# Optimization experiments

Measured on AMD Instinct MI355X. Metric: run time of the kernel, lower is better.

The kernel has to match this reference:

```python
import jax, jax.numpy as jnp
import numpy as np

B, N, P = 256, 12, 66
DN = 1024   # node_feature_size
DE = 1024   # edge_feature_size
D = 512     # message_size
DIMS = [3 * D, 1024, 512]  # shared trunk dims; heads differ only in out classes
C_LR, C_CR, C_MR = 9, 3, 5


def _mlp(x, Ws, bs):
    # ReLU MLP, no activation on final layer (eval mode: dropout is identity)
    for i, (W, b) in enumerate(zip(Ws, bs)):
        x = x @ W + b
        if i < len(Ws) - 1:
            x = jax.nn.relu(x)
    return x


def _head_params(key, out_dim):
    dims = DIMS + [out_dim]
    Ws, bs = [], []
    for i in range(len(dims) - 1):
        key, k = jax.random.split(key)
        Ws.append(jax.random.normal(k, (dims[i], dims[i + 1]), jnp.float32) * (1.0 / np.sqrt(dims[i])))
        bs.append(jnp.zeros((dims[i + 1],), jnp.float32))
    return Ws, bs


def setup_inputs() -> dict:
    key = jax.random.key(0)
    ks = jax.random.split(key, 12)
    inp = {
        'node_features': jax.random.normal(ks[0], (B, N, DN), jnp.float32),
        'edge_features': jax.random.normal(ks[1], (B, N, N, DE), jnp.float32),
        'edge_embeddings': jax.random.normal(ks[2], (B, N, N, D), jnp.float32),
        'pairs': jax.random.randint(ks[3], (B, P, 2), 0, N),
        'num_rels': jax.random.randint(ks[4], (B,), 0, P + 1),
        'W_node': jax.random.normal(ks[5], (DN, D), jnp.float32) * (1.0 / np.sqrt(DN)),
        'b_node': jnp.zeros((D,), jnp.float32),
        'W_edge': jax.random.normal(ks[6], (DE, D), jnp.float32) * (1.0 / np.sqrt(DE)),
        'b_edge': jnp.zeros((D,), jnp.float32),
    }
    for name, cdim, k in (('lr', C_LR, ks[7]), ('cr', C_CR, ks[8]), ('mr', C_MR, ks[9])):
        Ws, bs = _head_params(k, cdim)
        for i in range(3):
            inp[f'{name}_W{i}'] = Ws[i]
            inp[f'{name}_b{i}'] = bs[i]
    return inp


def reference(node_features, edge_features, edge_embeddings, pairs, num_rels,
              W_node, b_node, W_edge, b_edge,
              lr_W0, lr_b0, lr_W1, lr_b1, lr_W2, lr_b2,
              cr_W0, cr_b0, cr_W1, cr_b1, cr_W2, cr_b2,
              mr_W0, mr_b0, mr_W1, mr_b1, mr_W2, mr_b2):
    # feature resize linears
    nf = node_features @ W_node + b_node        # [B,N,D]
    ef = edge_features @ W_edge + b_edge        # [B,N,N,D]

    # vectorized make_classifier_inputs
    i0, i1 = pairs[..., 0], pairs[..., 1]       # [B,P]
    bidx = jnp.arange(nf.shape[0])[:, None]     # [B,1]
    n1 = nf[bidx, i0]                           # [B,P,D]
    n2 = nf[bidx, i1]                           # [B,P,D]
    emb_mean = 0.5 * (edge_embeddings[bidx, i0, i1] + edge_embeddings[bidx, i1, i0])
    feat_mean = 0.5 * (ef[bidx, i0, i1] + ef[bidx, i1, i0])
    e = 0.5 * (emb_mean + feat_mean)            # [B,P,D]
    ci = jnp.concatenate([n1, n2, e], axis=-1)  # [B,P,3D]

    # rows i >= num_rels[b] stay zero (preallocated-zeros semantics)
    valid = (jnp.arange(ci.shape[1])[None, :] < num_rels[:, None])[..., None]
    ci = jnp.where(valid, ci, jnp.zeros((), ci.dtype))

    lr = _mlp(ci, [lr_W0, lr_W1, lr_W2], [lr_b0, lr_b1, lr_b2])
    cr = _mlp(ci, [cr_W0, cr_W1, cr_W2], [cr_b0, cr_b1, cr_b2])
    mr = _mlp(ci, [mr_W0, mr_W1, mr_W2], [mr_b0, mr_b1, mr_b2])
    return lr, cr, mr
```

## Files before the change

### kernel.cpp

```cpp
#include <hip/hip_runtime.h>
#include <stdint.h>

#define BB 256
#define NNODE 12
#define PP 66
#define DNF 1024
#define DEF 1024
#define DD 512
#define MROWS (BB*PP)
#define MNODE (BB*NNODE)
#define MTILES (MROWS/128)

typedef __attribute__((ext_vector_type(8))) short s16x8;
typedef __attribute__((ext_vector_type(4))) float f32x4;
typedef __attribute__((ext_vector_type(8))) unsigned short u16x8;

__device__ __forceinline__ unsigned short f2bf(float f) {
  union { float f; unsigned u; } v; v.f = f;
  return (unsigned short)((v.u + 0x7FFFu + ((v.u >> 16) & 1u)) >> 16);
}
__device__ __forceinline__ float bf2f(unsigned short h) {
  union { unsigned u; float f; } v; v.u = ((unsigned)h) << 16;
  return v.f;
}

__device__ __forceinline__ void gll16(const void* g, void* l) {
  __builtin_amdgcn_global_load_lds(
      (const __attribute__((address_space(1))) void*)g,
      (__attribute__((address_space(3))) void*)l, 16, 0, 0);
}

__global__ __launch_bounds__(256) void k_front(
    const int* __restrict__ nrels, int* __restrict__ offs,
    int* __restrict__ Mv, int2* __restrict__ nodes,
    float* __restrict__ h1part,
    const float* __restrict__ node, unsigned short* __restrict__ node_bf,
    const float* __restrict__ W_node, unsigned short* __restrict__ WnT,
    const float* __restrict__ W_edge, unsigned short* __restrict__ WeT,
    const float* __restrict__ W0a, const float* __restrict__ W0b,
    const float* __restrict__ W0c, unsigned short* __restrict__ W0T,
    const float* __restrict__ W1a, const float* __restrict__ W1b,
    const float* __restrict__ W1c, unsigned short* __restrict__ W1T,
    const float* __restrict__ w2a, const float* __restrict__ w2b,
    const float* __restrict__ w2c,
    const float* __restrict__ b2a, const float* __restrict__ b2b,
    const float* __restrict__ b2c,
    unsigned short* __restrict__ W2T, float* __restrict__ b2pad,
    const float* __restrict__ b0a, const float* __restrict__ b0b,
    const float* __restrict__ b0c, float* __restrict__ b0cat,
    const float* __restrict__ b1a, const float* __restrict__ b1b,
    const float* __restrict__ b1c, float* __restrict__ b1cat,
    const float* __restrict__ b_node, const float* __restrict__ b_edge,
    float* __restrict__ b_ne) {
  __shared__ float tile[64][65];
  const int bid = blockIdx.x, t = threadIdx.x;
  if (bid < 24) {
    const int h = bid >> 3, c = bid & 7;
    const float* b0 = h == 0 ? b0a : (h == 1 ? b0b : b0c);
    const float* W1 = h == 0 ? W1a : (h == 1 ? W1b : W1c);
    const int k0 = c * 128;
    float acc0 = 0.f, acc1 = 0.f;
#pragma unroll 8
    for (int kk = 0; kk < 128; ++kk) {
      const int k = k0 + kk;
      const float bv = fmaxf(b0[k], 0.f);
      acc0 += bv * W1[(size_t)k * 512 + t];
      acc1 += bv * W1[(size_t)k * 512 + t + 256];
    }
    h1part[(size_t)bid * 512 + t] = acc0;
    h1part[(size_t)bid * 512 + t + 256] = acc1;
  } else if (bid == 24) {
    __shared__ int s[256];
    const int val = nrels[t];
    s[t] = val;
    __syncthreads();
    for (int d = 1; d < 256; d <<= 1) {
      int x = (t >= d) ? s[t - d] : 0;
      __syncthreads();
      s[t] += x;
      __syncthreads();
    }
    offs[t] = s[t] - val;
    __syncthreads();
    const int total = s[255];
    if (t == 0) *Mv = total;
    if (t < 128) {
      int cr = total + t;
      if (cr < MROWS) nodes[cr] = make_int2(0, 0);
    }
  } else if (bid < 3097) {
    int i = (bid - 25) * 256 + t;
    float4 v = ((const float4*)node)[i];
    ushort4 o;
    o.x = f2bf(v.x); o.y = f2bf(v.y); o.z = f2bf(v.z); o.w = f2bf(v.w);
    ((ushort4*)node_bf)[i] = o;
  } else if (bid < 4889) {
    int tau = bid - 3097;
    const float* src; unsigned short* dst; int K, N;
    if (tau < 128)       { src = W_node; dst = WnT; K = 1024; N = 512; }
    else if (tau < 256)  { src = W_edge; dst = WeT; K = 1024; N = 512; tau -= 128; }
    else if (tau < 1408) {
      int hh = (tau - 256) / 384; tau = (tau - 256) % 384;
      src = hh == 0 ? W0a : (hh == 1 ? W0b : W0c);
      dst = W0T + (size_t)hh * 1024 * 1536; K = 1536; N = 1024;
    } else {
      int hh = (tau - 1408) / 128; tau = (tau - 1408) % 128;
      src = hh == 0 ? W1a : (hh == 1 ? W1b : W1c);
      dst = W1T + (size_t)hh * 512 * 1024; K = 1024; N = 512;
    }
    const int ntn = N >> 6;
    const int kb = (tau / ntn) * 64, nb = (tau % ntn) * 64;
    const int tx = t & 15, ty = t >> 4;
#pragma unroll
    for (int i = 0; i < 4; i++) {
      float4 v = *(const float4*)&src[(size_t)(kb + ty + 16 * i) * N + nb + tx * 4];
      tile[ty + 16 * i][tx * 4 + 0] = v.x;
      tile[ty + 16 * i][tx * 4 + 1] = v.y;
      tile[ty + 16 * i][tx * 4 + 2] = v.z;
      tile[ty + 16 * i][tx * 4 + 3] = v.w;
    }
    __syncthreads();
    const int wx = t & 7, wy = t >> 3;
#pragma unroll
    for (int i = 0; i < 2; i++) {
      const int n = wy + 32 * i;
      u16x8 o;
#pragma unroll
      for (int j = 0; j < 8; j++) o[j] = f2bf(tile[wx * 8 + j][n]);
      *(u16x8*)&dst[(size_t)(nb + n) * K + kb + wx * 8] = o;
    }
  } else if (bid < 5657) {
    int e = bid - 4889;
    int h = e >> 8, blk = e & 255;
    const int C = (h == 0) ? 9 : ((h == 1) ? 3 : 5);
    const float* W2 = (h == 0) ? w2a : ((h == 1) ? w2b : w2c);
    const float* b2 = (h == 0) ? b2a : ((h == 1) ? b2b : b2c);
    int idx = blk * 256 + t;
    int n = idx >> 9, k = idx & 511;
    W2T[(size_t)h * 65536 + idx] = (n < C) ? f2bf(W2[(size_t)k * C + n]) : (unsigned short)0;
    if (blk == 0 && t < 128)
      b2pad[h * 128 + t] = (t < C) ? b2[t] : 0.f;
  } else if (bid < 5669) {
    int j = bid - 5657;
    const float* b0 = (j < 4) ? b0a : (j < 8 ? b0b : b0c);
    b0cat[j * 256 + t] = b0[(j & 3) * 256 + t];
  } else if (bid < 5675) {
    int j = bid - 5669;
    const float* b1 = (j < 2) ? b1a : (j < 4 ? b1b : b1c);
    b1cat[j * 256 + t] = b1[(j & 1) * 256 + t];
  } else {
    int idx = (bid - 5675) * 256 + t;
    b_ne[idx] = (idx < 512) ? b_node[idx] : b_edge[idx - 512];
  }
}

__global__ __launch_bounds__(256) void k_gather_fin(
    const float* __restrict__ EF, const float* __restrict__ EE,
    const int* __restrict__ pairs, const int* __restrict__ nrels,
    const int* __restrict__ offs,
    unsigned short* __restrict__ efm, unsigned short* __restrict__ emb,
    int2* __restrict__ nodes, int* __restrict__ rmap,
    const float* __restrict__ h1part,
    const float* __restrict__ b1a, const float* __restrict__ b1b,
    const float* __restrict__ b1c,
    const float* __restrict__ w2a, const float* __restrict__ w2b,
    const float* __restrict__ w2c,
    const float* __restrict__ b2a, const float* __restrict__ b2b,
    const float* __restrict__ b2c, float* __restrict__ outc) {
  const int bid = blockIdx.x, t = threadIdx.x;
  if (bid == MROWS) {
    __shared__ float red[9];
    for (int h = 0; h < 3; ++h) {
      const float* b1 = h == 0 ? b1a : (h == 1 ? b1b : b1c);
      const float* W2 = h == 0 ? w2a : (h == 1 ? w2b : w2c);
      const float* b2 = h == 0 ? b2a : (h == 1 ? b2b : b2c);
      const int C = h == 0 ? 9 : (h == 1 ? 3 : 5);
      const int obase = h == 0 ? 0 : (h == 1 ? 9 : 12);
      if (t < 9) red[t] = 0.f;
      float s0 = b1[t], s1 = b1[t + 256];
#pragma unroll
      for (int cc = 0; cc < 8; ++cc) {
        s0 += h1part[(size_t)(h * 8 + cc) * 512 + t];
        s1 += h1part[(size_t)(h * 8 + cc) * 512 + t + 256];
      }
      const float hv0 = fmaxf(s0, 0.f), hv1 = fmaxf(s1, 0.f);
      __syncthreads();
      float p[9] = {0.f, 0.f, 0.f, 0.f, 0.f, 0.f, 0.f, 0.f, 0.f};
#pragma unroll
      for (int c = 0; c < 9; ++c)
        if (c < C) p[c] = hv0 * W2[(size_t)t * C + c] + hv1 * W2[(size_t)(t + 256) * C + c];
#pragma unroll
      for (int c = 0; c < 9; ++c)
#pragma unroll
        for (int off = 32; off; off >>= 1) p[c] += __shfl_xor(p[c], off);
      if ((t & 63) == 0)
        for (int c = 0; c < C; ++c) atomicAdd(&red[c], p[c]);
      __syncthreads();
      if (t < C) outc[obase + t] = red[t] + b2[t];
      __syncthreads();
    }
    return;
  }
  int r = bid;
  int b = r / PP, p = r - b * PP;
  if (p >= nrels[b]) return;
  const int cr = offs[b] + p;
  int i0 = pairs[r * 2 + 0], i1 = pairs[r * 2 + 1];
  if (t == 0) {
    nodes[cr] = make_int2(b * NNODE + i0, b * NNODE + i1);
    rmap[cr] = r;
  }
  const float4* e01 = (const float4*)(EF + ((size_t)((b * NNODE + i0) * NNODE + i1)) * DEF);
  const float4* e10 = (const float4*)(EF + ((size_t)((b * NNODE + i1) * NNODE + i0)) * DEF);
  float4 a = e01[t], c = e10[t];
  ushort4 o;
  o.x = f2bf(0.5f * (a.x + c.x));
  o.y = f2bf(0.5f * (a.y + c.y));
  o.z = f2bf(0.5f * (a.z + c.z));
  o.w = f2bf(0.5f * (a.w + c.w));
  ((ushort4*)(efm + (size_t)cr * DEF))[t] = o;
  const float2* g01 = (const float2*)(EE + ((size_t)((b * NNODE + i0) * NNODE + i1)) * DD);
  const float2* g10 = (const float2*)(EE + ((size_t)((b * NNODE + i1) * NNODE + i0)) * DD);
  float2 x = g01[t], y = g10[t];
  ushort2 eo;
  eo.x = f2bf(0.25f * (x.x + y.x));
  eo.y = f2bf(0.25f * (x.y + y.y));
  ((ushort2*)(emb + (size_t)cr * DD))[t] = eo;
}

template <int EPI>
__global__ __launch_bounds__(256) void k_gemm(
    const unsigned short* __restrict__ A, int ldA,
    const unsigned short* __restrict__ BT, int ldB, int K,
    int Ntiles,
    const float* __restrict__ bias,
    unsigned short* __restrict__ outb, int ldo,
    const unsigned short* __restrict__ em,
    const int* __restrict__ Mvp,
    unsigned short* __restrict__ ci,
    int blocksPerHead, long long aHeadOff, long long bHeadOff,
    long long oHeadOff, int biasHeadOff,
    const int2* __restrict__ nodes,
    const unsigned short* __restrict__ nfa,
    const unsigned short* __restrict__ nfb,
    const int* __restrict__ rmap) {
  __shared__ __align__(16) unsigned short sm[16384];
  char* smc = (char*)sm;
  const int t = threadIdx.x;
  int bid = blockIdx.x;

  if constexpr (EPI == 6) {
    if (bid >= 2 * blocksPerHead) {
      const float* oc = (const float*)nfa;
      float* out = (float*)nfb;
      const int e = (bid - 2 * blocksPerHead) * 256 + t;
      if (e < MROWS * 17) {
        int c;
        if (e < MROWS * 9) c = e % 9;
        else if (e < MROWS * 12) c = 9 + (e - MROWS * 9) % 3;
        else c = 12 + (e - MROWS * 12) % 5;
        out[e] = oc[c];
      }
      return;
    }
  }

  const int l = t & 63, w = t >> 6;
  const int wm = w >> 1, wn = w & 1;

  int head = 0;
  unsigned short* outp = outb;
  if constexpr (EPI == 3) {
    head = bid / MTILES;
    bid -= head * MTILES;
    A += (size_t)head * MROWS * DD;
    BT += (size_t)head * 128 * DD;
    bias += head * 128;
  } else {
    if (blocksPerHead > 0) {
      head = bid / blocksPerHead;
      bid -= head * blocksPerHead;
      A += (long long)head * aHeadOff;
      BT += (long long)head * bHeadOff;
      bias += head * biasHeadOff;
      outp = outb + (long long)head * oHeadOff;
    }
  }
  const int tn = bid % Ntiles, tm = bid / Ntiles;

  int Mv = MROWS;
  if (Mvp) Mv = *Mvp;
  if constexpr (EPI == 6) { if (head == 0) Mv = MNODE; }
  if (Mvp) {
    if (tm * 128 >= Mv) return;
  }

  const int lrow = l >> 3;
  const int scol = (l & 7) ^ lrow;
  const unsigned short* Ap = A + (size_t)(tm * 128 + w * 8 + lrow) * ldA + scol * 8;
  const unsigned short* Bp = BT + (size_t)(tn * 128 + w * 8 + lrow) * ldB + scol * 8;

  f32x4 acc[4][4] = {};
  const int hi = l >> 4, l15 = l & 15, l7 = l & 7;
  const int nk = K >> 6;

  for (int kt = 0; kt < nk; ++kt) {
#pragma unroll
    for (int c = 0; c < 4; ++c) {
      gll16(Ap + (size_t)c * 32 * ldA, smc + c * 4096 + w * 1024);
      gll16(Bp + (size_t)c * 32 * ldB, smc + 16384 + c * 4096 + w * 1024);
    }
    __syncthreads();
#pragma unroll
    for (int kk = 0; kk < 2; ++kk) {
      const int cb = (((kk << 2) + hi) ^ l7) << 4;
      s16x8 af[4], bfr[4];
#pragma unroll
      for (int m = 0; m < 4; m++)
        af[m] = *(const s16x8*)(smc + (wm * 64 + m * 16 + l15) * 128 + cb);
#pragma unroll
      for (int n = 0; n < 4; n++)
        bfr[n] = *(const s16x8*)(smc + 16384 + (wn * 64 + n * 16 + l15) * 128 + cb);
#pragma unroll
      for (int m = 0; m < 4; m++)
#pragma unroll
        for (int n = 0; n < 4; n++)
          asm volatile("v_mfma_f32_16x16x32_bf16 %0, %1, %2, %0"
                       : "+v"(acc[m][n])
                       : "v"(af[m]), "v"(bfr[n]));
    }
    __syncthreads();
    Ap += 64;
    Bp += 64;
  }
  asm volatile("s_nop 7\n\ts_nop 7\n\ts_nop 7" :::);

  if constexpr (EPI == 5) {
    const int se_r = t >> 4;
    const int se_ch = t & 15;
#pragma unroll
    for (int it = 0; it < 8; ++it) {
      const int rr = se_r + (it << 4);
      const int2 nn = nodes[tm * 128 + rr];
      union { unsigned short s[8]; unsigned long long q[2]; } ov;
      u16x8 va = *(const u16x8*)&nfa[(size_t)nn.x * 3072 + tn * 128 + se_ch * 8];
      u16x8 vb = *(const u16x8*)&nfb[(size_t)nn.y * 3072 + tn * 128 + se_ch * 8];
#pragma unroll
      for (int j = 0; j < 8; ++j)
        ov.s[j] = f2bf(bf2f(va[j]) + bf2f(vb[j]));
      const int sch = se_ch ^ ((rr >> 2) & 7);
      *(unsigned long long*)(smc + rr * 256 + (sch << 4)) = ov.q[0];
      *(unsigned long long*)(smc + rr * 256 + (sch << 4) + 8) = ov.q[1];
    }
    __syncthreads();
  }

  const int gr_base = tm * 128 + wm * 64 + (hi << 2);
  const int gc_base = tn * 128 + wn * 64 + l15;
  const int lr_base = wm * 64 + (hi << 2);
  const int lc_base = wn * 64 + l15;

  int Cc = 0; size_t obase = 0;
  if constexpr (EPI == 3) {
    Cc = (head == 0) ? 9 : ((head == 1) ? 3 : 5);
    obase = (head == 0) ? 0 : ((head == 1) ? (size_t)MROWS * 9 : (size_t)MROWS * 12);
  }

#pragma unroll
  for (int n = 0; n < 4; n++) {
    const int gc = gc_base + n * 16;
    const float bv = (EPI == 4) ? 0.f : bias[gc];
#pragma unroll
    for (int m = 0; m < 4; m++) {
#pragma unroll
      for (int i = 0; i < 4; i++) {
        const int gr = gr_base + m * 16 + i;
        float v = acc[m][n][i] + bv;
        if constexpr (EPI == 0 || EPI == 4) {
          outp[(size_t)gr * ldo + gc] = f2bf(v);
        } else if constexpr (EPI == 2) {
          outp[(size_t)gr * ldo + gc] = f2bf(v > 0.f ? v : 0.f);
        } else if constexpr (EPI == 5) {
          const int lr = lr_base + m * 16 + i;
          const int lc = lc_base + n * 16;
          const int rch = (lc >> 3) ^ ((lr >> 2) & 7);
          v += bf2f(*(const unsigned short*)(smc + lr * 256 + (rch << 4) + (lc & 7) * 2));
          outp[(size_t)gr * ldo + gc] = f2bf(v > 0.f ? v : 0.f);
        } else if constexpr (EPI == 6) {
          if (head == 0) {
            outp[(size_t)gr * ldo + gc] = f2bf(v);
          } else {
            float e = bf2f(em[(size_t)gr * DD + gc]) + 0.5f * v;
            ci[(size_t)gr * DD + gc] = f2bf(e);
          }
        } else {
          if (gc < Cc && gr < Mv)
            ((float*)outb)[obase + (size_t)rmap[gr] * Cc + gc] = v;
        }
      }
    }
  }
}

extern "C" void kernel_launch(void* const* d_in, const int* in_sizes, int n_in,
                              void* d_out, int out_size, void* d_ws, size_t ws_size,
                              hipStream_t stream) {
  const float* node   = (const float*)d_in[0];
  const float* EF     = (const float*)d_in[1];
  const float* EE     = (const float*)d_in[2];
  const int*   pairs  = (const int*)d_in[3];
  const int*   nrels  = (const int*)d_in[4];
  const float* W_node = (const float*)d_in[5];
  const float* b_node = (const float*)d_in[6];
  const float* W_edge = (const float*)d_in[7];
  const float* b_edge = (const float*)d_in[8];
  const float* hW0[3] = {(const float*)d_in[9],  (const float*)d_in[15], (const float*)d_in[21]};
  const float* hb0[3] = {(const float*)d_in[10], (const float*)d_in[16], (const float*)d_in[22]};
  const float* hW1[3] = {(const float*)d_in[11], (const float*)d_in[17], (const float*)d_in[23]};
  const float* hb1[3] = {(const float*)d_in[12], (const float*)d_in[18], (const float*)d_in[24]};
  const float* hW2[3] = {(const float*)d_in[13], (const float*)d_in[19], (const float*)d_in[25]};
  const float* hb2[3] = {(const float*)d_in[14], (const float*)d_in[20], (const float*)d_in[26]};

  char* ws = (char*)d_ws;
  size_t off = 0;
  auto alloc = [&](size_t bytes) {
    char* p = ws + off;
    off += (bytes + 255) & ~(size_t)255;
    return p;
  };
  unsigned short* WnT    = (unsigned short*)alloc((size_t)512 * 1024 * 2);
  unsigned short* WeT    = (unsigned short*)alloc((size_t)512 * 1024 * 2);
  unsigned short* W0T    = (unsigned short*)alloc((size_t)3072 * 1536 * 2);
  unsigned short* W1T    = (unsigned short*)alloc((size_t)3 * 512 * 1024 * 2);
  unsigned short* W2T    = (unsigned short*)alloc((size_t)3 * 128 * 512 * 2);
  float*          b2pad  = (float*)alloc((size_t)3 * 128 * 4);
  float*          b0cat  = (float*)alloc((size_t)3072 * 4);
  float*          b1cat  = (float*)alloc((size_t)1536 * 4);
  float*          b_ne   = (float*)alloc((size_t)1024 * 4);
  int2*           nodes  = (int2*)alloc((size_t)MROWS * 8);
  int*            offs   = (int*)alloc((size_t)256 * 4);
  int*            Mv     = (int*)alloc(256);
  int*            rmap   = (int*)alloc((size_t)MROWS * 4);
  float*          outc   = (float*)alloc((size_t)32 * 4);
  float*          h1part = (float*)alloc((size_t)24 * 512 * 4);
  size_t zoneA = off;
  unsigned short* efm = (unsigned short*)alloc((size_t)MROWS * DEF * 2);
  unsigned short* EMb = (unsigned short*)alloc((size_t)MROWS * DD * 2);
  unsigned short* ci_e = (unsigned short*)alloc((size_t)MROWS * DD * 2);
  size_t zoneC = off;
  unsigned short* node_bf = (unsigned short*)alloc((size_t)MNODE * DNF * 2);
  unsigned short* nf      = (unsigned short*)alloc((size_t)MNODE * DD * 2);
  unsigned short* nfa   = (unsigned short*)(ws + zoneA);
  unsigned short* nfb   = nfa + (size_t)MNODE * 3072;
  unsigned short* h1    = (unsigned short*)(ws + zoneA);
  unsigned short* h0big = (unsigned short*)(ws + zoneC);

  k_front<<<5679, 256, 0, stream>>>(nrels, offs, Mv, nodes, h1part,
      node, node_bf, W_node, WnT, W_edge, WeT,
      hW0[0], hW0[1], hW0[2], W0T, hW1[0], hW1[1], hW1[2], W1T,
      hW2[0], hW2[1], hW2[2], hb2[0], hb2[1], hb2[2], W2T, b2pad,
      hb0[0], hb0[1], hb0[2], b0cat, hb1[0], hb1[1], hb1[2], b1cat,
      b_node, b_edge, b_ne);
  k_gather_fin<<<MROWS + 1, 256, 0, stream>>>(EF, EE, pairs, nrels, offs,
      efm, EMb, nodes, rmap, h1part,
      hb1[0], hb1[1], hb1[2], hW2[0], hW2[1], hW2[2],
      hb2[0], hb2[1], hb2[2], outc);

  k_gemm<6><<<2 * MTILES * 4 + (MROWS * 17 + 255) / 256, 256, 0, stream>>>(
      node_bf, 1024, WnT, 1024, 1024, 4, b_ne, nf, 512,
      EMb, Mv, ci_e, MTILES * 4,
      (long long)(efm - node_bf), (long long)512 * 1024,
      (long long)(ci_e - nf), 512,
      nullptr, (const unsigned short*)outc, (const unsigned short*)d_out, nullptr);

  k_gemm<4><<<2 * (MNODE / 128) * 24, 256, 0, stream>>>(
      nf, 512, W0T, 1536, 512, 24, nullptr, nfa, 3072,
      nullptr, nullptr, nullptr, (MNODE / 128) * 24,
      0, 512, (long long)MNODE * 3072, 0, nullptr, nullptr, nullptr, nullptr);

  k_gemm<5><<<MTILES * 24, 256, 0, stream>>>(
      ci_e, 512, W0T + 1024, 1536, 512, 24, b0cat, h0big, 3072,
      nullptr, Mv, nullptr, 0, 0, 0, 0, 0, nodes, nfa, nfb, nullptr);

  k_gemm<2><<<3 * MTILES * 4, 256, 0, stream>>>(
      h0big, 3072, W1T, 1024, 1024, 4, b1cat, h1, 512,
      nullptr, Mv, nullptr, MTILES * 4,
      1024, (long long)512 * 1024, (long long)MROWS * DD, 512,
      nullptr, nullptr, nullptr, nullptr);

  k_gemm<3><<<3 * MTILES, 256, 0, stream>>>(
      h1, 512, W2T, 512, 512, 1, b2pad, (unsigned short*)d_out, 0,
      nullptr, Mv, nullptr, 0, 0, 0, 0, 0, nullptr, nullptr, nullptr, rmap);
}
```

Before: 201.4 us.

## Fuse node-resize GEMM into gather kernel and merge edge and W0 node GEMMs

```diff
diff --git a/kernel.cpp b/kernel.cpp
--- a/kernel.cpp
+++ b/kernel.cpp
@@ -154,7 +154,158 @@
   }
 }
 
-__global__ __launch_bounds__(256) void k_gather_fin(
+template <int EPI>
+__device__ __forceinline__ void gemm_body(
+    unsigned short* sm,
+    const unsigned short* __restrict__ A, int ldA,
+    const unsigned short* __restrict__ BT, int ldB, int K,
+    int Ntiles,
+    const float* __restrict__ bias,
+    unsigned short* __restrict__ outb, int ldo,
+    const unsigned short* __restrict__ em,
+    const int* __restrict__ Mvp,
+    unsigned short* __restrict__ ci,
+    int blocksPerHead, long long aHeadOff, long long bHeadOff,
+    long long oHeadOff, int biasHeadOff,
+    const int2* __restrict__ nodes,
+    const unsigned short* __restrict__ nfa,
+    const unsigned short* __restrict__ nfb,
+    const int* __restrict__ rmap, int bid) {
+  char* smc = (char*)sm;
+  const int t = threadIdx.x;
+  const int l = t & 63, w = t >> 6;
+  const int wm = w >> 1, wn = w & 1;
+
+  int head = 0;
+  unsigned short* outp = outb;
+  if constexpr (EPI == 3) {
+    head = bid / MTILES;
+    bid -= head * MTILES;
+    A += (size_t)head * MROWS * DD;
+    BT += (size_t)head * 128 * DD;
+    bias += head * 128;
+  } else {
+    if (blocksPerHead > 0) {
+      head = bid / blocksPerHead;
+      bid -= head * blocksPerHead;
+      A += (long long)head * aHeadOff;
+      BT += (long long)head * bHeadOff;
+      bias += head * biasHeadOff;
+      outp = outb + (long long)head * oHeadOff;
+    }
+  }
+  const int tn = bid % Ntiles, tm = bid / Ntiles;
+
+  int Mv = MROWS;
+  if (Mvp) {
+    Mv = *Mvp;
+    if (tm * 128 >= Mv) return;
+  }
+
+  const int lrow = l >> 3;
+  const int scol = (l & 7) ^ lrow;
+  const unsigned short* Ap = A + (size_t)(tm * 128 + w * 8 + lrow) * ldA + scol * 8;
+  const unsigned short* Bp = BT + (size_t)(tn * 128 + w * 8 + lrow) * ldB + scol * 8;
+
+  f32x4 acc[4][4] = {};
+  const int hi = l >> 4, l15 = l & 15, l7 = l & 7;
+  const int nk = K >> 6;
+
+  for (int kt = 0; kt < nk; ++kt) {
+#pragma unroll
+    for (int c = 0; c < 4; ++c) {
+      gll16(Ap + (size_t)c * 32 * ldA, smc + c * 4096 + w * 1024);
+      gll16(Bp + (size_t)c * 32 * ldB, smc + 16384 + c * 4096 + w * 1024);
+    }
+    __syncthreads();
+#pragma unroll
+    for (int kk = 0; kk < 2; ++kk) {
+      const int cb = (((kk << 2) + hi) ^ l7) << 4;
+      s16x8 af[4], bfr[4];
+#pragma unroll
+      for (int m = 0; m < 4; m++)
+        af[m] = *(const s16x8*)(smc + (wm * 64 + m * 16 + l15) * 128 + cb);
+#pragma unroll
+      for (int n = 0; n < 4; n++)
+        bfr[n] = *(const s16x8*)(smc + 16384 + (wn * 64 + n * 16 + l15) * 128 + cb);
+#pragma unroll
+      for (int m = 0; m < 4; m++)
+#pragma unroll
+        for (int n = 0; n < 4; n++)
+          asm volatile("v_mfma_f32_16x16x32_bf16 %0, %1, %2, %0"
+                       : "+v"(acc[m][n])
+                       : "v"(af[m]), "v"(bfr[n]));
+    }
+    __syncthreads();
+    Ap += 64;
+    Bp += 64;
+  }
+  asm volatile("s_nop 7\n\ts_nop 7\n\ts_nop 7" :::);
+
+  if constexpr (EPI == 5) {
+    const int se_r = t >> 4;
+    const int se_ch = t & 15;
+#pragma unroll
+    for (int it = 0; it < 8; ++it) {
+      const int rr = se_r + (it << 4);
+      const int2 nn = nodes[tm * 128 + rr];
+      union { unsigned short s[8]; unsigned long long q[2]; } ov;
+      u16x8 va = *(const u16x8*)&nfa[(size_t)nn.x * 3072 + tn * 128 + se_ch * 8];
+      u16x8 vb = *(const u16x8*)&nfb[(size_t)nn.y * 3072 + tn * 128 + se_ch * 8];
+#pragma unroll
+      for (int j = 0; j < 8; ++j)
+        ov.s[j] = f2bf(bf2f(va[j]) + bf2f(vb[j]));
+      const int sch = se_ch ^ ((rr >> 2) & 7);
+      *(unsigned long long*)(smc + rr * 256 + (sch << 4)) = ov.q[0];
+      *(unsigned long long*)(smc + rr * 256 + (sch << 4) + 8) = ov.q[1];
+    }
+    __syncthreads();
+  }
+
+  const int gr_base = tm * 128 + wm * 64 + (hi << 2);
+  const int gc_base = tn * 128 + wn * 64 + l15;
+  const int lr_base = wm * 64 + (hi << 2);
+  const int lc_base = wn * 64 + l15;
+
+  int Cc = 0; size_t obase = 0;
+  if constexpr (EPI == 3) {
+    Cc = (head == 0) ? 9 : ((head == 1) ? 3 : 5);
+    obase = (head == 0) ? 0 : ((head == 1) ? (size_t)MROWS * 9 : (size_t)MROWS * 12);
+  }
+
+#pragma unroll
+  for (int n = 0; n < 4; n++) {
+    const int gc = gc_base + n * 16;
+    const float bv = (EPI == 4) ? 0.f : bias[gc];
+#pragma unroll
+    for (int m = 0; m < 4; m++) {
+#pragma unroll
+      for (int i = 0; i < 4; i++) {
+        const int gr = gr_base + m * 16 + i;
+        float v = acc[m][n][i] + bv;
+        if constexpr (EPI == 0 || EPI == 4) {
+          outp[(size_t)gr * ldo + gc] = f2bf(v);
+        } else if constexpr (EPI == 1) {
+          float e = bf2f(em[(size_t)gr * DD + gc]) + 0.5f * v;
+          ci[(size_t)gr * DD + gc] = f2bf(e);
+        } else if constexpr (EPI == 2) {
+          outp[(size_t)gr * ldo + gc] = f2bf(v > 0.f ? v : 0.f);
+        } else if constexpr (EPI == 5) {
+          const int lr = lr_base + m * 16 + i;
+          const int lc = lc_base + n * 16;
+          const int rch = (lc >> 3) ^ ((lr >> 2) & 7);
+          v += bf2f(*(const unsigned short*)(smc + lr * 256 + (rch << 4) + (lc & 7) * 2));
+          outp[(size_t)gr * ldo + gc] = f2bf(v > 0.f ? v : 0.f);
+        } else {
+          if (gc < Cc && gr < Mv)
+            ((float*)outb)[obase + (size_t)rmap[gr] * Cc + gc] = v;
+        }
+      }
+    }
+  }
+}
+
+__global__ __launch_bounds__(256) void k_gather_nf(
     const float* __restrict__ EF, const float* __restrict__ EE,
     const int* __restrict__ pairs, const int* __restrict__ nrels,
     const int* __restrict__ offs,
@@ -166,10 +317,20 @@
     const float* __restrict__ w2a, const float* __restrict__ w2b,
     const float* __restrict__ w2c,
     const float* __restrict__ b2a, const float* __restrict__ b2b,
-    const float* __restrict__ b2c, float* __restrict__ outc) {
+    const float* __restrict__ b2c, float* __restrict__ outc,
+    const unsigned short* __restrict__ node_bf,
+    const unsigned short* __restrict__ WnT,
+    const float* __restrict__ b_node, unsigned short* __restrict__ nf) {
+  __shared__ __align__(16) unsigned short sm[16384];
   const int bid = blockIdx.x, t = threadIdx.x;
+  if (bid > MROWS) {
+    gemm_body<0>(sm, node_bf, 1024, WnT, 1024, 1024, 4, b_node, nf, 512,
+                 nullptr, nullptr, nullptr, 0, 0, 0, 0, 0,
+                 nullptr, nullptr, nullptr, nullptr, bid - MROWS - 1);
+    return;
+  }
   if (bid == MROWS) {
-    __shared__ float red[9];
+    float* red = (float*)sm;
     for (int h = 0; h < 3; ++h) {
       const float* b1 = h == 0 ? b1a : (h == 1 ? b1b : b1c);
       const float* W2 = h == 0 ? w2a : (h == 1 ? w2b : w2c);
@@ -226,6 +387,37 @@
   eo.x = f2bf(0.25f * (x.x + y.x));
   eo.y = f2bf(0.25f * (x.y + y.y));
   ((ushort2*)(emb + (size_t)cr * DD))[t] = eo;
+}
+
+__global__ __launch_bounds__(256) void k_mid(
+    const unsigned short* __restrict__ efm, const unsigned short* __restrict__ WeT,
+    const float* __restrict__ b_edge,
+    const unsigned short* __restrict__ EMb, const int* __restrict__ Mvp,
+    unsigned short* __restrict__ ci_e,
+    const unsigned short* __restrict__ nf, const unsigned short* __restrict__ W0T,
+    unsigned short* __restrict__ nfa,
+    const float* __restrict__ outc, float* __restrict__ out) {
+  __shared__ __align__(16) unsigned short sm[16384];
+  const int bid = blockIdx.x, t = threadIdx.x;
+  if (bid < 528) {
+    gemm_body<1>(sm, efm, 1024, WeT, 1024, 1024, 4, b_edge, nullptr, 0,
+                 EMb, Mvp, ci_e, 0, 0, 0, 0, 0,
+                 nullptr, nullptr, nullptr, nullptr, bid);
+  } else if (bid < 1680) {
+    gemm_body<4>(sm, nf, 512, W0T, 1536, 512, 24, nullptr, nfa, 3072,
+                 nullptr, nullptr, nullptr, 576,
+                 0, 512, (long long)MNODE * 3072, 0,
+                 nullptr, nullptr, nullptr, nullptr, bid - 528);
+  } else {
+    const int e = (bid - 1680) * 256 + t;
+    if (e < MROWS * 17) {
+      int c;
+      if (e < MROWS * 9) c = e % 9;
+      else if (e < MROWS * 12) c = 9 + (e - MROWS * 9) % 3;
+      else c = 12 + (e - MROWS * 12) % 5;
+      out[e] = outc[c];
+    }
+  }
 }
 
 template <int EPI>
@@ -245,161 +437,9 @@
     const unsigned short* __restrict__ nfb,
     const int* __restrict__ rmap) {
   __shared__ __align__(16) unsigned short sm[16384];
-  char* smc = (char*)sm;
-  const int t = threadIdx.x;
-  int bid = blockIdx.x;
-
-  if constexpr (EPI == 6) {
-    if (bid >= 2 * blocksPerHead) {
-      const float* oc = (const float*)nfa;
-      float* out = (float*)nfb;
-      const int e = (bid - 2 * blocksPerHead) * 256 + t;
-      if (e < MROWS * 17) {
-        int c;
-        if (e < MROWS * 9) c = e % 9;
-        else if (e < MROWS * 12) c = 9 + (e - MROWS * 9) % 3;
-        else c = 12 + (e - MROWS * 12) % 5;
-        out[e] = oc[c];
-      }
-      return;
-    }
-  }
-
-  const int l = t & 63, w = t >> 6;
-  const int wm = w >> 1, wn = w & 1;
-
-  int head = 0;
-  unsigned short* outp = outb;
-  if constexpr (EPI == 3) {
-    head = bid / MTILES;
-    bid -= head * MTILES;
-    A += (size_t)head * MROWS * DD;
-    BT += (size_t)head * 128 * DD;
-    bias += head * 128;
-  } else {
-    if (blocksPerHead > 0) {
-      head = bid / blocksPerHead;
-      bid -= head * blocksPerHead;
-      A += (long long)head * aHeadOff;
-      BT += (long long)head * bHeadOff;
-      bias += head * biasHeadOff;
-      outp = outb + (long long)head * oHeadOff;
-    }
-  }
-  const int tn = bid % Ntiles, tm = bid / Ntiles;
-
-  int Mv = MROWS;
-  if (Mvp) Mv = *Mvp;
-  if constexpr (EPI == 6) { if (head == 0) Mv = MNODE; }
-  if (Mvp) {
-    if (tm * 128 >= Mv) return;
-  }
-
-  const int lrow = l >> 3;
-  const int scol = (l & 7) ^ lrow;
-  const unsigned short* Ap = A + (size_t)(tm * 128 + w * 8 + lrow) * ldA + scol * 8;
-  const unsigned short* Bp = BT + (size_t)(tn * 128 + w * 8 + lrow) * ldB + scol * 8;
-
-  f32x4 acc[4][4] = {};
-  const int hi = l >> 4, l15 = l & 15, l7 = l & 7;
-  const int nk = K >> 6;
-
-  for (int kt = 0; kt < nk; ++kt) {
-#pragma unroll
-    for (int c = 0; c < 4; ++c) {
-      gll16(Ap + (size_t)c * 32 * ldA, smc + c * 4096 + w * 1024);
-      gll16(Bp + (size_t)c * 32 * ldB, smc + 16384 + c * 4096 + w * 1024);
-    }
-    __syncthreads();
-#pragma unroll
-    for (int kk = 0; kk < 2; ++kk) {
-      const int cb = (((kk << 2) + hi) ^ l7) << 4;
-      s16x8 af[4], bfr[4];
-#pragma unroll
-      for (int m = 0; m < 4; m++)
-        af[m] = *(const s16x8*)(smc + (wm * 64 + m * 16 + l15) * 128 + cb);
-#pragma unroll
-      for (int n = 0; n < 4; n++)
-        bfr[n] = *(const s16x8*)(smc + 16384 + (wn * 64 + n * 16 + l15) * 128 + cb);
-#pragma unroll
-      for (int m = 0; m < 4; m++)
-#pragma unroll
-        for (int n = 0; n < 4; n++)
-          asm volatile("v_mfma_f32_16x16x32_bf16 %0, %1, %2, %0"
-                       : "+v"(acc[m][n])
-                       : "v"(af[m]), "v"(bfr[n]));
-    }
-    __syncthreads();
-    Ap += 64;
-    Bp += 64;
-  }
-  asm volatile("s_nop 7\n\ts_nop 7\n\ts_nop 7" :::);
-
-  if constexpr (EPI == 5) {
-    const int se_r = t >> 4;
-    const int se_ch = t & 15;
-#pragma unroll
-    for (int it = 0; it < 8; ++it) {
-      const int rr = se_r + (it << 4);
-      const int2 nn = nodes[tm * 128 + rr];
-      union { unsigned short s[8]; unsigned long long q[2]; } ov;
-      u16x8 va = *(const u16x8*)&nfa[(size_t)nn.x * 3072 + tn * 128 + se_ch * 8];
-      u16x8 vb = *(const u16x8*)&nfb[(size_t)nn.y * 3072 + tn * 128 + se_ch * 8];
-#pragma unroll
-      for (int j = 0; j < 8; ++j)
-        ov.s[j] = f2bf(bf2f(va[j]) + bf2f(vb[j]));
-      const int sch = se_ch ^ ((rr >> 2) & 7);
-      *(unsigned long long*)(smc + rr * 256 + (sch << 4)) = ov.q[0];
-      *(unsigned long long*)(smc + rr * 256 + (sch << 4) + 8) = ov.q[1];
-    }
-    __syncthreads();
-  }
-
-  const int gr_base = tm * 128 + wm * 64 + (hi << 2);
-  const int gc_base = tn * 128 + wn * 64 + l15;
-  const int lr_base = wm * 64 + (hi << 2);
-  const int lc_base = wn * 64 + l15;
-
-  int Cc = 0; size_t obase = 0;
-  if constexpr (EPI == 3) {
-    Cc = (head == 0) ? 9 : ((head == 1) ? 3 : 5);
-    obase = (head == 0) ? 0 : ((head == 1) ? (size_t)MROWS * 9 : (size_t)MROWS * 12);
-  }
-
-#pragma unroll
-  for (int n = 0; n < 4; n++) {
-    const int gc = gc_base + n * 16;
-    const float bv = (EPI == 4) ? 0.f : bias[gc];
-#pragma unroll
-    for (int m = 0; m < 4; m++) {
-#pragma unroll
-      for (int i = 0; i < 4; i++) {
-        const int gr = gr_base + m * 16 + i;
-        float v = acc[m][n][i] + bv;
-        if constexpr (EPI == 0 || EPI == 4) {
-          outp[(size_t)gr * ldo + gc] = f2bf(v);
-        } else if constexpr (EPI == 2) {
-          outp[(size_t)gr * ldo + gc] = f2bf(v > 0.f ? v : 0.f);
-        } else if constexpr (EPI == 5) {
-          const int lr = lr_base + m * 16 + i;
-          const int lc = lc_base + n * 16;
-          const int rch = (lc >> 3) ^ ((lr >> 2) & 7);
-          v += bf2f(*(const unsigned short*)(smc + lr * 256 + (rch << 4) + (lc & 7) * 2));
-          outp[(size_t)gr * ldo + gc] = f2bf(v > 0.f ? v : 0.f);
-        } else if constexpr (EPI == 6) {
-          if (head == 0) {
-            outp[(size_t)gr * ldo + gc] = f2bf(v);
-          } else {
-            float e = bf2f(em[(size_t)gr * DD + gc]) + 0.5f * v;
-            ci[(size_t)gr * DD + gc] = f2bf(e);
-          }
-        } else {
-          if (gc < Cc && gr < Mv)
-            ((float*)outb)[obase + (size_t)rmap[gr] * Cc + gc] = v;
-        }
-      }
-    }
-  }
+  gemm_body<EPI>(sm, A, ldA, BT, ldB, K, Ntiles, bias, outb, ldo, em, Mvp, ci,
+                 blocksPerHead, aHeadOff, bHeadOff, oHeadOff, biasHeadOff,
+                 nodes, nfa, nfb, rmap, blockIdx.x);
 }
 
 extern "C" void kernel_launch(void* const* d_in, const int* in_sizes, int n_in,
@@ -443,16 +483,16 @@
   int*            rmap   = (int*)alloc((size_t)MROWS * 4);
   float*          outc   = (float*)alloc((size_t)32 * 4);
   float*          h1part = (float*)alloc((size_t)24 * 512 * 4);
-  size_t zoneA = off;
-  unsigned short* efm = (unsigned short*)alloc((size_t)MROWS * DEF * 2);
-  unsigned short* EMb = (unsigned short*)alloc((size_t)MROWS * DD * 2);
+  size_t zoneB = off;
   unsigned short* ci_e = (unsigned short*)alloc((size_t)MROWS * DD * 2);
+  unsigned short* nfa  = (unsigned short*)alloc((size_t)MNODE * 3072 * 2);
+  unsigned short* nfb  = (unsigned short*)alloc((size_t)MNODE * 3072 * 2);
   size_t zoneC = off;
   unsigned short* node_bf = (unsigned short*)alloc((size_t)MNODE * DNF * 2);
   unsigned short* nf      = (unsigned short*)alloc((size_t)MNODE * DD * 2);
-  unsigned short* nfa   = (unsigned short*)(ws + zoneA);
-  unsigned short* nfb   = nfa + (size_t)MNODE * 3072;
-  unsigned short* h1    = (unsigned short*)(ws + zoneA);
+  unsigned short* efm     = (unsigned short*)alloc((size_t)MROWS * DEF * 2);
+  unsigned short* EMb     = (unsigned short*)alloc((size_t)MROWS * DD * 2);
+  unsigned short* h1    = (unsigned short*)(ws + zoneB);
   unsigned short* h0big = (unsigned short*)(ws + zoneC);
 
   k_front<<<5679, 256, 0, stream>>>(nrels, offs, Mv, nodes, h1part,
@@ -461,22 +501,16 @@
       hW2[0], hW2[1], hW2[2], hb2[0], hb2[1], hb2[2], W2T, b2pad,
       hb0[0], hb0[1], hb0[2], b0cat, hb1[0], hb1[1], hb1[2], b1cat,
       b_node, b_edge, b_ne);
-  k_gather_fin<<<MROWS + 1, 256, 0, stream>>>(EF, EE, pairs, nrels, offs,
-      efm, EMb, nodes, rmap, h1part,
+
+  k_gather_nf<<<MROWS + 1 + (MNODE / 128) * 4, 256, 0, stream>>>(
+      EF, EE, pairs, nrels, offs, efm, EMb, nodes, rmap, h1part,
       hb1[0], hb1[1], hb1[2], hW2[0], hW2[1], hW2[2],
-      hb2[0], hb2[1], hb2[2], outc);
-
-  k_gemm<6><<<2 * MTILES * 4 + (MROWS * 17 + 255) / 256, 256, 0, stream>>>(
-      node_bf, 1024, WnT, 1024, 1024, 4, b_ne, nf, 512,
-      EMb, Mv, ci_e, MTILES * 4,
-      (long long)(efm - node_bf), (long long)512 * 1024,
-      (long long)(ci_e - nf), 512,
-      nullptr, (const unsigned short*)outc, (const unsigned short*)d_out, nullptr);
-
-  k_gemm<4><<<2 * (MNODE / 128) * 24, 256, 0, stream>>>(
-      nf, 512, W0T, 1536, 512, 24, nullptr, nfa, 3072,
-      nullptr, nullptr, nullptr, (MNODE / 128) * 24,
-      0, 512, (long long)MNODE * 3072, 0, nullptr, nullptr, nullptr, nullptr);
+      hb2[0], hb2[1], hb2[2], outc,
+      node_bf, WnT, b_ne, nf);
+
+  k_mid<<<1680 + (MROWS * 17 + 255) / 256, 256, 0, stream>>>(
+      efm, WeT, b_ne + 512, EMb, Mv, ci_e,
+      nf, W0T, nfa, outc, (float*)d_out);
 
   k_gemm<5><<<MTILES * 24, 256, 0, stream>>>(
       ci_e, 512, W0T + 1024, 1536, 512, 24, b0cat, h0big, 3072,
```

Measured after the change: 198.8 us. No clear change (-1.3%).
